# Optimization experiments

Measured on AMD Instinct MI355X. Metric: run time of the kernel, lower is better.

The kernel has to match this reference:

```python
import jax, jax.numpy as jnp
import numpy as np

D_IN = 128
D_OUT = 128
B, N = 8, 2048
NEG = -9e15


def setup_inputs() -> dict:
    key = jax.random.key(0)
    ks = jax.random.split(key, 7)
    x = jax.random.normal(ks[0], (B, N, D_IN), dtype=jnp.float32)
    adj = jax.random.randint(ks[1], (B, N, N), 0, 2).astype(jnp.float32)
    s_in = 1.0 / np.sqrt(D_IN)
    s_out = 1.0 / np.sqrt(D_OUT)
    s_g = 1.0 / np.sqrt(2 * D_OUT)
    # torch.nn.Linear weights stored pre-transposed: [in, out]
    W_w = jax.random.uniform(ks[2], (D_IN, D_OUT), jnp.float32, -s_in, s_in)
    W_b = jax.random.uniform(ks[3], (D_OUT,), jnp.float32, -s_in, s_in)
    A_w = jax.random.uniform(ks[4], (D_OUT, D_OUT), jnp.float32, -s_out, s_out)
    gate_w = jax.random.uniform(ks[5], (2 * D_OUT, 1), jnp.float32, -s_g, s_g)
    gate_b = jax.random.uniform(ks[6], (1,), jnp.float32, -s_g, s_g)
    return {"x": x, "adj": adj, "W_w": W_w, "W_b": W_b, "A_w": A_w,
            "gate_w": gate_w, "gate_b": gate_b}


def reference(x, adj, W_w, W_b, A_w, gate_w, gate_b):
    h = x @ W_w + W_b                                  # [B,N,D]
    e = jnp.einsum('bnd,bmd->bnm', h @ A_w, h)          # [B,N,N]
    e = e + jnp.swapaxes(e, 1, 2)                       # symmetric
    att = jnp.where(adj > 0, e, NEG)
    att = jax.nn.softmax(att, axis=1)                   # NOTE: dim=1 as in torch code
    att = att * adj
    h_prime = jax.nn.relu(jnp.einsum('bnm,bmd->bnd', att, h))
    coeff = jax.nn.sigmoid(jnp.concatenate([x, h_prime], axis=-1) @ gate_w + gate_b)  # [B,N,1]
    return coeff * x + (1.0 - coeff) * h_prime
```

## Files before the change

### kernel.cpp

```cpp
#include <hip/hip_runtime.h>
#include <hip/hip_bf16.h>

#define B_ 8
#define N_ 2048
#define D_ 128

typedef __bf16 bf16_t;
typedef __bf16 v8bf __attribute__((ext_vector_type(8)));
typedef float  v4f  __attribute__((ext_vector_type(4)));

__global__ __launch_bounds__(256) void k_prep(
    const float* __restrict__ Ww, const float* __restrict__ Aw,
    bf16_t* __restrict__ WT, bf16_t* __restrict__ AT)
{
    int idx = blockIdx.x * 256 + threadIdx.x;
    int o = idx >> 7, i = idx & 127;
    WT[idx] = (bf16_t)Ww[i * D_ + o];
    AT[idx] = (bf16_t)Aw[i * D_ + o];
}

__global__ __launch_bounds__(256) void k_hg(
    const float* __restrict__ x, const float* __restrict__ Wb,
    const bf16_t* __restrict__ WT, const bf16_t* __restrict__ AT,
    bf16_t* __restrict__ hb, bf16_t* __restrict__ gb)
{
    int wave = threadIdx.x >> 6;
    int lane = threadIdx.x & 63;
    int q = lane >> 4;
    int c = lane & 15;
    int nrow0 = blockIdx.x * 64 + wave * 16;

    __shared__ float pw_all[4][16][132];
    float (*pw)[132] = pw_all[wave];

    v8bf ax[4];
#pragma unroll
    for (int kc = 0; kc < 4; ++kc) {
        const float* src = x + (size_t)(nrow0 + c) * D_ + kc * 32 + q * 8;
        float4 f0 = *(const float4*)src;
        float4 f1 = *(const float4*)(src + 4);
        v8bf a;
        a[0]=(bf16_t)f0.x; a[1]=(bf16_t)f0.y; a[2]=(bf16_t)f0.z; a[3]=(bf16_t)f0.w;
        a[4]=(bf16_t)f1.x; a[5]=(bf16_t)f1.y; a[6]=(bf16_t)f1.z; a[7]=(bf16_t)f1.w;
        ax[kc] = a;
    }

#pragma unroll
    for (int ct = 0; ct < 8; ++ct) {
        float bias = Wb[ct * 16 + c];
        v4f acc = {bias, bias, bias, bias};
#pragma unroll
        for (int kc = 0; kc < 4; ++kc) {
            v8bf bw = *(const v8bf*)(WT + (size_t)(ct * 16 + c) * D_ + kc * 32 + q * 8);
            acc = __builtin_amdgcn_mfma_f32_16x16x32_bf16(ax[kc], bw, acc, 0, 0, 0);
        }
#pragma unroll
        for (int r = 0; r < 4; ++r) pw[q * 4 + r][ct * 16 + c] = acc[r];
    }
    __builtin_amdgcn_wave_barrier();

    v8bf ahf[4];
#pragma unroll
    for (int kc = 0; kc < 4; ++kc) {
        v4f p0 = *(const v4f*)&pw[c][kc * 32 + q * 8];
        v4f p1 = *(const v4f*)&pw[c][kc * 32 + q * 8 + 4];
        v8bf a;
#pragma unroll
        for (int j = 0; j < 4; ++j) { a[j] = (bf16_t)p0[j]; a[j+4] = (bf16_t)p1[j]; }
        ahf[kc] = a;
    }
    {
        int row = lane >> 2, seg = lane & 3;
#pragma unroll
        for (int v = 0; v < 4; ++v) {
            v8bf hv;
#pragma unroll
            for (int j = 0; j < 8; ++j) hv[j] = (bf16_t)pw[row][seg * 32 + v * 8 + j];
            *(v8bf*)(hb + (size_t)(nrow0 + row) * D_ + seg * 32 + v * 8) = hv;
        }
    }
    __builtin_amdgcn_wave_barrier();

#pragma unroll
    for (int ct = 0; ct < 8; ++ct) {
        v4f acc = {0.f, 0.f, 0.f, 0.f};
#pragma unroll
        for (int kc = 0; kc < 4; ++kc) {
            v8bf bw = *(const v8bf*)(AT + (size_t)(ct * 16 + c) * D_ + kc * 32 + q * 8);
            acc = __builtin_amdgcn_mfma_f32_16x16x32_bf16(ahf[kc], bw, acc, 0, 0, 0);
        }
#pragma unroll
        for (int r = 0; r < 4; ++r) pw[q * 4 + r][ct * 16 + c] = acc[r];
    }
    __builtin_amdgcn_wave_barrier();
    {
        int row = lane >> 2, seg = lane & 3;
#pragma unroll
        for (int v = 0; v < 4; ++v) {
            v8bf gv;
#pragma unroll
            for (int j = 0; j < 8; ++j) gv[j] = (bf16_t)pw[row][seg * 32 + v * 8 + j];
            *(v8bf*)(gb + (size_t)(nrow0 + row) * D_ + seg * 32 + v * 8) = gv;
        }
    }
}

__global__ __launch_bounds__(256, 4) void k_att(
    const bf16_t* __restrict__ hb, const bf16_t* __restrict__ gb,
    const float* __restrict__ adj, float* __restrict__ colsum,
    bf16_t* __restrict__ Pt)
{
    int bid = blockIdx.x;
    int b = bid & 7;
    int rest = bid >> 3;
    int nblk = rest >> 3;
    int mgrp = rest & 7;
    int wave = threadIdx.x >> 6;
    int lane = threadIdx.x & 63;
    int q = lane >> 4;
    int c = lane & 15;
    int nbase = nblk * 32;
    int mwav = mgrp * 256 + wave * 64;
    const size_t hgoff = (size_t)b * N_ * D_;
    const float* adjb = adj + (size_t)b * N_ * N_;

    __shared__ __align__(16) bf16_t eb_all[4][32][72];
    bf16_t (*eb)[72] = eb_all[wave];

    v8bf ag[2][4], ah[2][4];
#pragma unroll
    for (int sub = 0; sub < 2; ++sub)
#pragma unroll
        for (int kc = 0; kc < 4; ++kc) {
            size_t off = hgoff + (size_t)(nbase + sub * 16 + c) * D_ + kc * 32 + q * 8;
            ag[sub][kc] = *(const v8bf*)(gb + off);
            ah[sub][kc] = *(const v8bf*)(hb + off);
        }

    for (int t = 0; t < 4; ++t) {
        int mt = mwav + t * 16;
        float av[2][4];
#pragma unroll
        for (int sub = 0; sub < 2; ++sub)
#pragma unroll
            for (int r = 0; r < 4; ++r)
                av[sub][r] = adjb[(size_t)(nbase + sub * 16 + q * 4 + r) * N_ + mt + c];
        v8bf bh[4], bg[4];
#pragma unroll
        for (int kc = 0; kc < 4; ++kc) {
            size_t off = hgoff + (size_t)(mt + c) * D_ + kc * 32 + q * 8;
            bh[kc] = *(const v8bf*)(hb + off);
            bg[kc] = *(const v8bf*)(gb + off);
        }
        v4f e[2];
        e[0] = (v4f){0.f, 0.f, 0.f, 0.f};
        e[1] = (v4f){0.f, 0.f, 0.f, 0.f};
#pragma unroll
        for (int kc = 0; kc < 4; ++kc)
#pragma unroll
            for (int sub = 0; sub < 2; ++sub) {
                e[sub] = __builtin_amdgcn_mfma_f32_16x16x32_bf16(ag[sub][kc], bh[kc], e[sub], 0, 0, 0);
                e[sub] = __builtin_amdgcn_mfma_f32_16x16x32_bf16(ah[sub][kc], bg[kc], e[sub], 0, 0, 0);
            }
        float cs = 0.f;
#pragma unroll
        for (int sub = 0; sub < 2; ++sub)
#pragma unroll
            for (int r = 0; r < 4; ++r) {
                float ex = __expf(e[sub][r]);
                float pv = (av[sub][r] > 0.f) ? ex : 0.f;
                eb[sub * 16 + q * 4 + r][t * 16 + c] = (bf16_t)pv;
                cs += pv;
            }
        cs += __shfl_xor(cs, 16);
        cs += __shfl_xor(cs, 32);
        if (lane < 16) atomicAdd(&colsum[b * N_ + mt + lane], cs);
    }
    __builtin_amdgcn_wave_barrier();
    int prow = lane >> 3, pseg = lane & 7;
#pragma unroll
    for (int pass = 0; pass < 4; ++pass) {
        int row = pass * 8 + prow;
        v8bf o = *(const v8bf*)&eb[row][pseg * 8];
        *(v8bf*)(Pt + ((size_t)b * N_ + nbase + row) * N_ + mwav + pseg * 8) = o;
    }
}

__global__ __launch_bounds__(256) void k_scaleT(
    const bf16_t* __restrict__ hb, const float* __restrict__ colsum,
    bf16_t* __restrict__ hbTs)
{
    int bid = blockIdx.x;
    int b = bid >> 6;
    int rem = bid & 63;
    int nblk = rem >> 1;
    int dblk = rem & 1;
    int tid = threadIdx.x;
    __shared__ bf16_t sm[64][72];
    __shared__ float sinv[64];
    int n0 = nblk * 64, d0 = dblk * 64;
    int r = tid >> 3, cg = tid & 7;
#pragma unroll
    for (int rr = 0; rr < 2; ++rr) {
        int row = r + rr * 32;
        *(v8bf*)&sm[row][cg * 8] =
            *(const v8bf*)(hb + (size_t)(b * N_ + n0 + row) * D_ + d0 + cg * 8);
    }
    if (tid < 64) {
        float s = colsum[b * N_ + n0 + tid];
        sinv[tid] = (s > 0.f) ? 1.f / s : 0.f;
    }
    __syncthreads();
#pragma unroll
    for (int rr = 0; rr < 2; ++rr) {
        int dr = r + rr * 32;
        v8bf v;
#pragma unroll
        for (int jj = 0; jj < 8; ++jj)
            v[jj] = (bf16_t)((float)sm[cg * 8 + jj][dr] * sinv[cg * 8 + jj]);
        *(v8bf*)(hbTs + (size_t)(b * D_ + d0 + dr) * N_ + n0 + cg * 8) = v;
    }
}

__global__ __launch_bounds__(512, 4) void k_out(
    const bf16_t* __restrict__ Pt, const bf16_t* __restrict__ hbTs,
    const float* __restrict__ x, const float* __restrict__ gw,
    const float* __restrict__ gbias, float* __restrict__ out)
{
    int bid = blockIdx.x;
    int b = bid & 7;
    int nblk = bid >> 3;
    int tid = threadIdx.x;
    int wave = tid >> 6;
    int lane = tid & 63;
    int q = lane >> 4;
    int c = lane & 15;
    int nbase = nblk * 32;
    int m0 = wave * 256;

    __shared__ float hp[32][132];

    const bf16_t* hTb = hbTs + (size_t)b * D_ * N_;
    const bf16_t* Pb  = Pt + (size_t)b * N_ * N_;

    v4f acc[2][8];
#pragma unroll
    for (int sub = 0; sub < 2; ++sub)
#pragma unroll
        for (int dt = 0; dt < 8; ++dt) acc[sub][dt] = (v4f){0.f, 0.f, 0.f, 0.f};

    for (int ch = 0; ch < 8; ++ch) {
        int mch = m0 + ch * 32;
        v8bf a[2];
#pragma unroll
        for (int sub = 0; sub < 2; ++sub)
            a[sub] = *(const v8bf*)(Pb + (size_t)(nbase + sub * 16 + c) * N_ + mch + q * 8);
        v8bf vt[8];
#pragma unroll
        for (int dt = 0; dt < 8; ++dt)
            vt[dt] = *(const v8bf*)(hTb + (size_t)(dt * 16 + c) * N_ + mch + q * 8);
#pragma unroll
        for (int dt = 0; dt < 8; ++dt)
#pragma unroll
            for (int sub = 0; sub < 2; ++sub)
                acc[sub][dt] = __builtin_amdgcn_mfma_f32_16x16x32_bf16(a[sub], vt[dt], acc[sub][dt], 0, 0, 0);
    }

    if (wave == 0) {
#pragma unroll
        for (int sub = 0; sub < 2; ++sub)
#pragma unroll
            for (int dt = 0; dt < 8; ++dt)
#pragma unroll
                for (int r = 0; r < 4; ++r)
                    hp[sub * 16 + q * 4 + r][dt * 16 + c] = acc[sub][dt][r];
    }
    __syncthreads();
#pragma unroll
    for (int wv = 1; wv < 8; ++wv) {
        if (wave == wv) {
#pragma unroll
            for (int sub = 0; sub < 2; ++sub)
#pragma unroll
                for (int dt = 0; dt < 8; ++dt)
#pragma unroll
                    for (int r = 0; r < 4; ++r)
                        hp[sub * 16 + q * 4 + r][dt * 16 + c] += acc[sub][dt][r];
        }
        __syncthreads();
    }

    int row = tid >> 4;
    int seg = tid & 15;
    size_t g = (size_t)b * N_ + nbase + row;
    const float* xr = x + g * D_ + seg * 8;
    float4 xa = *(const float4*)xr;
    float4 xb = *(const float4*)(xr + 4);
    float hv[8];
#pragma unroll
    for (int j = 0; j < 8; ++j) hv[j] = fmaxf(hp[row][seg * 8 + j], 0.f);
    float part = xa.x * gw[seg*8+0] + xa.y * gw[seg*8+1] + xa.z * gw[seg*8+2] + xa.w * gw[seg*8+3]
               + xb.x * gw[seg*8+4] + xb.y * gw[seg*8+5] + xb.z * gw[seg*8+6] + xb.w * gw[seg*8+7];
#pragma unroll
    for (int j = 0; j < 8; ++j) part += hv[j] * gw[D_ + seg * 8 + j];
    part += __shfl_xor(part, 1);
    part += __shfl_xor(part, 2);
    part += __shfl_xor(part, 4);
    part += __shfl_xor(part, 8);
    float coeff = 1.f / (1.f + __expf(-(part + gbias[0])));
    float4 o0, o1;
    o0.x = coeff * xa.x + (1.f - coeff) * hv[0];
    o0.y = coeff * xa.y + (1.f - coeff) * hv[1];
    o0.z = coeff * xa.z + (1.f - coeff) * hv[2];
    o0.w = coeff * xa.w + (1.f - coeff) * hv[3];
    o1.x = coeff * xb.x + (1.f - coeff) * hv[4];
    o1.y = coeff * xb.y + (1.f - coeff) * hv[5];
    o1.z = coeff * xb.z + (1.f - coeff) * hv[6];
    o1.w = coeff * xb.w + (1.f - coeff) * hv[7];
    float* orow = out + g * D_ + seg * 8;
    *(float4*)orow = o0;
    *(float4*)(orow + 4) = o1;
}

extern "C" void kernel_launch(void* const* d_in, const int* in_sizes, int n_in,
                              void* d_out, int out_size, void* d_ws, size_t ws_size,
                              hipStream_t stream)
{
    const float* x     = (const float*)d_in[0];
    const float* adj   = (const float*)d_in[1];
    const float* Ww    = (const float*)d_in[2];
    const float* Wb    = (const float*)d_in[3];
    const float* Aw    = (const float*)d_in[4];
    const float* gw    = (const float*)d_in[5];
    const float* gbias = (const float*)d_in[6];
    float* out = (float*)d_out;

    char* ws = (char*)d_ws;
    bf16_t* hb     = (bf16_t*)(ws);
    bf16_t* gb     = (bf16_t*)(ws + (4 << 20));
    bf16_t* hbTs   = (bf16_t*)(ws + (8 << 20));
    float*  colsum = (float*)(ws + (12 << 20));
    bf16_t* Pt     = (bf16_t*)(ws + (17 << 20));
    bf16_t* WT     = (bf16_t*)(ws + (81 << 20));
    bf16_t* AT     = (bf16_t*)(ws + (81 << 20) + (32 << 10));

    hipMemsetAsync(colsum, 0, B_ * N_ * sizeof(float), stream);
    k_prep<<<64, 256, 0, stream>>>(Ww, Aw, WT, AT);
    k_hg<<<B_ * N_ / 64, 256, 0, stream>>>(x, Wb, WT, AT, hb, gb);
    k_att<<<4096, 256, 0, stream>>>(hb, gb, adj, colsum, Pt);
    k_scaleT<<<512, 256, 0, stream>>>(hb, colsum, hbTs);
    k_out<<<512, 512, 0, stream>>>(Pt, hbTs, x, gw, gbias, out);
}
```

Baseline: 358.9 us.

## Enlarge attention tile, prefetch B operands, and coalesce adjacency loads

Each block now covers 64 n-rows instead of 32, so every loaded column tile of h/g feeds twice as many MFMAs and the grid halves. The next m-tile's h/g operands are prefetched into registers while the current tile computes. Adjacency masking and column-sum accumulation move into the write-out phase, which reads adj as float4 in coalesced rows and makes fewer, wider atomic adds. The cost is more registers per thread (launch bounds lowered to 2 blocks per SM) and twice the shared memory, so occupancy drops.

```diff
diff --git a/kernel.cpp b/kernel.cpp
--- a/kernel.cpp
+++ b/kernel.cpp
@@ -8,6 +8,9 @@
 typedef __bf16 bf16_t;
 typedef __bf16 v8bf __attribute__((ext_vector_type(8)));
 typedef float  v4f  __attribute__((ext_vector_type(4)));
+
+template <typename T>
+__device__ __forceinline__ void pinv(T& x) { asm volatile("" : "+v"(x)); }
 
 __global__ __launch_bounds__(256) void k_prep(
     const float* __restrict__ Ww, const float* __restrict__ Aw,
@@ -105,7 +108,7 @@
     }
 }
 
-__global__ __launch_bounds__(256, 4) void k_att(
+__global__ __launch_bounds__(256, 2) void k_att(
     const bf16_t* __restrict__ hb, const bf16_t* __restrict__ gb,
     const float* __restrict__ adj, float* __restrict__ colsum,
     bf16_t* __restrict__ Pt)
@@ -119,70 +122,97 @@
     int lane = threadIdx.x & 63;
     int q = lane >> 4;
     int c = lane & 15;
-    int nbase = nblk * 32;
+    int nbase = nblk * 64;
     int mwav = mgrp * 256 + wave * 64;
     const size_t hgoff = (size_t)b * N_ * D_;
     const float* adjb = adj + (size_t)b * N_ * N_;
 
-    __shared__ __align__(16) bf16_t eb_all[4][32][72];
+    __shared__ __align__(16) bf16_t eb_all[4][64][72];
     bf16_t (*eb)[72] = eb_all[wave];
 
-    v8bf ag[2][4], ah[2][4];
-#pragma unroll
-    for (int sub = 0; sub < 2; ++sub)
+    v8bf ag[4][4], ah[4][4];
+#pragma unroll
+    for (int sub = 0; sub < 4; ++sub)
 #pragma unroll
         for (int kc = 0; kc < 4; ++kc) {
             size_t off = hgoff + (size_t)(nbase + sub * 16 + c) * D_ + kc * 32 + q * 8;
             ag[sub][kc] = *(const v8bf*)(gb + off);
             ah[sub][kc] = *(const v8bf*)(hb + off);
         }
+#pragma unroll
+    for (int sub = 0; sub < 4; ++sub)
+#pragma unroll
+        for (int kc = 0; kc < 4; ++kc) { pinv(ag[sub][kc]); pinv(ah[sub][kc]); }
+
+    v8bf bh[4], bg[4], bhn[4], bgn[4];
+#pragma unroll
+    for (int kc = 0; kc < 4; ++kc) {
+        size_t off = hgoff + (size_t)(mwav + c) * D_ + kc * 32 + q * 8;
+        bh[kc] = *(const v8bf*)(hb + off);
+        bg[kc] = *(const v8bf*)(gb + off);
+    }
 
     for (int t = 0; t < 4; ++t) {
-        int mt = mwav + t * 16;
-        float av[2][4];
-#pragma unroll
-        for (int sub = 0; sub < 2; ++sub)
-#pragma unroll
-            for (int r = 0; r < 4; ++r)
-                av[sub][r] = adjb[(size_t)(nbase + sub * 16 + q * 4 + r) * N_ + mt + c];
-        v8bf bh[4], bg[4];
-#pragma unroll
-        for (int kc = 0; kc < 4; ++kc) {
-            size_t off = hgoff + (size_t)(mt + c) * D_ + kc * 32 + q * 8;
-            bh[kc] = *(const v8bf*)(hb + off);
-            bg[kc] = *(const v8bf*)(gb + off);
-        }
-        v4f e[2];
-        e[0] = (v4f){0.f, 0.f, 0.f, 0.f};
-        e[1] = (v4f){0.f, 0.f, 0.f, 0.f};
+        if (t < 3) {
+            int mt = mwav + (t + 1) * 16;
+#pragma unroll
+            for (int kc = 0; kc < 4; ++kc) {
+                size_t off = hgoff + (size_t)(mt + c) * D_ + kc * 32 + q * 8;
+                bhn[kc] = *(const v8bf*)(hb + off);
+                bgn[kc] = *(const v8bf*)(gb + off);
+            }
+        }
+        v4f e[4];
+#pragma unroll
+        for (int sub = 0; sub < 4; ++sub) e[sub] = (v4f){0.f, 0.f, 0.f, 0.f};
 #pragma unroll
         for (int kc = 0; kc < 4; ++kc)
 #pragma unroll
-            for (int sub = 0; sub < 2; ++sub) {
+            for (int sub = 0; sub < 4; ++sub) {
                 e[sub] = __builtin_amdgcn_mfma_f32_16x16x32_bf16(ag[sub][kc], bh[kc], e[sub], 0, 0, 0);
                 e[sub] = __builtin_amdgcn_mfma_f32_16x16x32_bf16(ah[sub][kc], bg[kc], e[sub], 0, 0, 0);
             }
-        float cs = 0.f;
-#pragma unroll
-        for (int sub = 0; sub < 2; ++sub)
-#pragma unroll
-            for (int r = 0; r < 4; ++r) {
-                float ex = __expf(e[sub][r]);
-                float pv = (av[sub][r] > 0.f) ? ex : 0.f;
-                eb[sub * 16 + q * 4 + r][t * 16 + c] = (bf16_t)pv;
-                cs += pv;
-            }
-        cs += __shfl_xor(cs, 16);
-        cs += __shfl_xor(cs, 32);
-        if (lane < 16) atomicAdd(&colsum[b * N_ + mt + lane], cs);
+#pragma unroll
+        for (int sub = 0; sub < 4; ++sub)
+#pragma unroll
+            for (int r = 0; r < 4; ++r)
+                eb[sub * 16 + q * 4 + r][t * 16 + c] = (bf16_t)__expf(e[sub][r]);
+#pragma unroll
+        for (int kc = 0; kc < 4; ++kc) { bh[kc] = bhn[kc]; bg[kc] = bgn[kc]; }
     }
     __builtin_amdgcn_wave_barrier();
+
     int prow = lane >> 3, pseg = lane & 7;
-#pragma unroll
-    for (int pass = 0; pass < 4; ++pass) {
+    float cs[8];
+#pragma unroll
+    for (int j = 0; j < 8; ++j) cs[j] = 0.f;
+#pragma unroll
+    for (int pass = 0; pass < 8; ++pass) {
         int row = pass * 8 + prow;
-        v8bf o = *(const v8bf*)&eb[row][pseg * 8];
+        v8bf e8 = *(const v8bf*)&eb[row][pseg * 8];
+        const float* ap = adjb + (size_t)(nbase + row) * N_ + mwav + pseg * 8;
+        float4 a0 = *(const float4*)ap;
+        float4 a1 = *(const float4*)(ap + 4);
+        float am[8] = {a0.x, a0.y, a0.z, a0.w, a1.x, a1.y, a1.z, a1.w};
+        v8bf o;
+#pragma unroll
+        for (int j = 0; j < 8; ++j) {
+            bool live = am[j] > 0.f;
+            o[j] = live ? e8[j] : (bf16_t)0.f;
+            cs[j] += live ? (float)e8[j] : 0.f;
+        }
         *(v8bf*)(Pt + ((size_t)b * N_ + nbase + row) * N_ + mwav + pseg * 8) = o;
+    }
+#pragma unroll
+    for (int j = 0; j < 8; ++j) {
+        cs[j] += __shfl_xor(cs[j], 8);
+        cs[j] += __shfl_xor(cs[j], 16);
+        cs[j] += __shfl_xor(cs[j], 32);
+    }
+    if (lane < 8) {
+#pragma unroll
+        for (int j = 0; j < 8; ++j)
+            atomicAdd(&colsum[b * N_ + mwav + lane * 8 + j], cs[j]);
     }
 }
 
@@ -347,7 +377,7 @@
     hipMemsetAsync(colsum, 0, B_ * N_ * sizeof(float), stream);
     k_prep<<<64, 256, 0, stream>>>(Ww, Aw, WT, AT);
     k_hg<<<B_ * N_ / 64, 256, 0, stream>>>(x, Wb, WT, AT, hb, gb);
-    k_att<<<4096, 256, 0, stream>>>(hb, gb, adj, colsum, Pt);
+    k_att<<<2048, 256, 0, stream>>>(hb, gb, adj, colsum, Pt);
     k_scaleT<<<512, 256, 0, stream>>>(hb, colsum, hbTs);
     k_out<<<512, 512, 0, stream>>>(Pt, hbTs, x, gw, gbias, out);
 }
```

Result: faster. 332.1 us (-7.5%).

## Double k_att row tile with LDS-staged operands and prefetch next column tile

Applied to the files above, without the earlier changes.

k_att now handles 64 n-rows per block instead of 32, stages those rows' h and g tiles in shared memory, and prefetches the next 16-column h/g fragment while computing the current one. This halves the grid and reuses each loaded m-side fragment across more rows, at the cost of LDS reads inside the MFMA loop and lower occupancy (launch bounds 4 to 3). Pt is now written directly from registers as scattered 2-byte stores rather than via an LDS transpose with 16-byte stores, which may hurt write coalescing. k_hg is also restructured into 512-thread blocks of 32 rows, with waves splitting the output columns and block-level syncs.

```diff
diff --git a/kernel.cpp b/kernel.cpp
--- a/kernel.cpp
+++ b/kernel.cpp
@@ -19,24 +19,27 @@
     AT[idx] = (bf16_t)Aw[i * D_ + o];
 }
 
-__global__ __launch_bounds__(256) void k_hg(
+__global__ __launch_bounds__(512) void k_hg(
     const float* __restrict__ x, const float* __restrict__ Wb,
     const bf16_t* __restrict__ WT, const bf16_t* __restrict__ AT,
     bf16_t* __restrict__ hb, bf16_t* __restrict__ gb)
 {
-    int wave = threadIdx.x >> 6;
-    int lane = threadIdx.x & 63;
+    int tid = threadIdx.x;
+    int lane = tid & 63;
+    int wave = tid >> 6;
     int q = lane >> 4;
     int c = lane & 15;
-    int nrow0 = blockIdx.x * 64 + wave * 16;
-
-    __shared__ float pw_all[4][16][132];
-    float (*pw)[132] = pw_all[wave];
+    int rg = wave & 1;
+    int dh = wave >> 1;
+    int row0 = blockIdx.x * 32;
+    int nrow = row0 + rg * 16;
+
+    __shared__ float hs[32][132];
 
     v8bf ax[4];
 #pragma unroll
     for (int kc = 0; kc < 4; ++kc) {
-        const float* src = x + (size_t)(nrow0 + c) * D_ + kc * 32 + q * 8;
+        const float* src = x + (size_t)(nrow + c) * D_ + kc * 32 + q * 8;
         float4 f0 = *(const float4*)src;
         float4 f1 = *(const float4*)(src + 4);
         v8bf a;
@@ -46,7 +49,8 @@
     }
 
 #pragma unroll
-    for (int ct = 0; ct < 8; ++ct) {
+    for (int t = 0; t < 2; ++t) {
+        int ct = dh * 2 + t;
         float bias = Wb[ct * 16 + c];
         v4f acc = {bias, bias, bias, bias};
 #pragma unroll
@@ -55,57 +59,62 @@
             acc = __builtin_amdgcn_mfma_f32_16x16x32_bf16(ax[kc], bw, acc, 0, 0, 0);
         }
 #pragma unroll
-        for (int r = 0; r < 4; ++r) pw[q * 4 + r][ct * 16 + c] = acc[r];
-    }
-    __builtin_amdgcn_wave_barrier();
+        for (int r = 0; r < 4; ++r) hs[rg * 16 + q * 4 + r][ct * 16 + c] = acc[r];
+    }
+    __syncthreads();
 
     v8bf ahf[4];
 #pragma unroll
     for (int kc = 0; kc < 4; ++kc) {
-        v4f p0 = *(const v4f*)&pw[c][kc * 32 + q * 8];
-        v4f p1 = *(const v4f*)&pw[c][kc * 32 + q * 8 + 4];
+        v4f p0 = *(const v4f*)&hs[rg * 16 + c][kc * 32 + q * 8];
+        v4f p1 = *(const v4f*)&hs[rg * 16 + c][kc * 32 + q * 8 + 4];
         v8bf a;
 #pragma unroll
         for (int j = 0; j < 4; ++j) { a[j] = (bf16_t)p0[j]; a[j+4] = (bf16_t)p1[j]; }
         ahf[kc] = a;
     }
     {
-        int row = lane >> 2, seg = lane & 3;
-#pragma unroll
-        for (int v = 0; v < 4; ++v) {
-            v8bf hv;
-#pragma unroll
-            for (int j = 0; j < 8; ++j) hv[j] = (bf16_t)pw[row][seg * 32 + v * 8 + j];
-            *(v8bf*)(hb + (size_t)(nrow0 + row) * D_ + seg * 32 + v * 8) = hv;
-        }
-    }
-    __builtin_amdgcn_wave_barrier();
-
-#pragma unroll
-    for (int ct = 0; ct < 8; ++ct) {
+        int r2 = tid >> 4, s = tid & 15;
+        v4f p0 = *(const v4f*)&hs[r2][s * 8];
+        v4f p1 = *(const v4f*)&hs[r2][s * 8 + 4];
+        v8bf hv;
+#pragma unroll
+        for (int j = 0; j < 4; ++j) { hv[j] = (bf16_t)p0[j]; hv[j+4] = (bf16_t)p1[j]; }
+        *(v8bf*)(hb + (size_t)(row0 + r2) * D_ + s * 8) = hv;
+    }
+
+    v4f gacc[2];
+#pragma unroll
+    for (int t = 0; t < 2; ++t) {
+        int ct = dh * 2 + t;
         v4f acc = {0.f, 0.f, 0.f, 0.f};
 #pragma unroll
         for (int kc = 0; kc < 4; ++kc) {
             v8bf bw = *(const v8bf*)(AT + (size_t)(ct * 16 + c) * D_ + kc * 32 + q * 8);
             acc = __builtin_amdgcn_mfma_f32_16x16x32_bf16(ahf[kc], bw, acc, 0, 0, 0);
         }
-#pragma unroll
-        for (int r = 0; r < 4; ++r) pw[q * 4 + r][ct * 16 + c] = acc[r];
-    }
-    __builtin_amdgcn_wave_barrier();
+        gacc[t] = acc;
+    }
+    __syncthreads();
+#pragma unroll
+    for (int t = 0; t < 2; ++t) {
+        int ct = dh * 2 + t;
+#pragma unroll
+        for (int r = 0; r < 4; ++r) hs[rg * 16 + q * 4 + r][ct * 16 + c] = gacc[t][r];
+    }
+    __syncthreads();
     {
-        int row = lane >> 2, seg = lane & 3;
-#pragma unroll
-        for (int v = 0; v < 4; ++v) {
-            v8bf gv;
-#pragma unroll
-            for (int j = 0; j < 8; ++j) gv[j] = (bf16_t)pw[row][seg * 32 + v * 8 + j];
-            *(v8bf*)(gb + (size_t)(nrow0 + row) * D_ + seg * 32 + v * 8) = gv;
-        }
-    }
-}
-
-__global__ __launch_bounds__(256, 4) void k_att(
+        int r2 = tid >> 4, s = tid & 15;
+        v4f p0 = *(const v4f*)&hs[r2][s * 8];
+        v4f p1 = *(const v4f*)&hs[r2][s * 8 + 4];
+        v8bf gv;
+#pragma unroll
+        for (int j = 0; j < 4; ++j) { gv[j] = (bf16_t)p0[j]; gv[j+4] = (bf16_t)p1[j]; }
+        *(v8bf*)(gb + (size_t)(row0 + r2) * D_ + s * 8) = gv;
+    }
+}
+
+__global__ __launch_bounds__(256, 3) void k_att(
     const bf16_t* __restrict__ hb, const bf16_t* __restrict__ gb,
     const float* __restrict__ adj, float* __restrict__ colsum,
     bf16_t* __restrict__ Pt)
@@ -115,74 +124,82 @@
     int rest = bid >> 3;
     int nblk = rest >> 3;
     int mgrp = rest & 7;
-    int wave = threadIdx.x >> 6;
-    int lane = threadIdx.x & 63;
+    int tid = threadIdx.x;
+    int wave = tid >> 6;
+    int lane = tid & 63;
     int q = lane >> 4;
     int c = lane & 15;
-    int nbase = nblk * 32;
+    int nbase = nblk * 64;
     int mwav = mgrp * 256 + wave * 64;
     const size_t hgoff = (size_t)b * N_ * D_;
     const float* adjb = adj + (size_t)b * N_ * N_;
 
-    __shared__ __align__(16) bf16_t eb_all[4][32][72];
-    bf16_t (*eb)[72] = eb_all[wave];
-
-    v8bf ag[2][4], ah[2][4];
-#pragma unroll
-    for (int sub = 0; sub < 2; ++sub)
-#pragma unroll
-        for (int kc = 0; kc < 4; ++kc) {
-            size_t off = hgoff + (size_t)(nbase + sub * 16 + c) * D_ + kc * 32 + q * 8;
-            ag[sub][kc] = *(const v8bf*)(gb + off);
-            ah[sub][kc] = *(const v8bf*)(hb + off);
-        }
+    __shared__ __align__(16) bf16_t hs[64][136];
+    __shared__ __align__(16) bf16_t gs[64][136];
+
+    {
+        int r = tid >> 2, seg = tid & 3;
+        const bf16_t* hsrc = hb + hgoff + (size_t)(nbase + r) * D_ + seg * 32;
+        const bf16_t* gsrc = gb + hgoff + (size_t)(nbase + r) * D_ + seg * 32;
+#pragma unroll
+        for (int v = 0; v < 4; ++v) {
+            *(v8bf*)&hs[r][seg * 32 + v * 8] = *(const v8bf*)(hsrc + v * 8);
+            *(v8bf*)&gs[r][seg * 32 + v * 8] = *(const v8bf*)(gsrc + v * 8);
+        }
+    }
+    __syncthreads();
+
+    v8bf bh[4], bg[4], bhn[4], bgn[4];
+#pragma unroll
+    for (int kc = 0; kc < 4; ++kc) {
+        size_t off = hgoff + (size_t)(mwav + c) * D_ + kc * 32 + q * 8;
+        bh[kc] = *(const v8bf*)(hb + off);
+        bg[kc] = *(const v8bf*)(gb + off);
+    }
 
     for (int t = 0; t < 4; ++t) {
         int mt = mwav + t * 16;
-        float av[2][4];
-#pragma unroll
-        for (int sub = 0; sub < 2; ++sub)
+        float av[4][4];
+#pragma unroll
+        for (int sub = 0; sub < 4; ++sub)
 #pragma unroll
             for (int r = 0; r < 4; ++r)
                 av[sub][r] = adjb[(size_t)(nbase + sub * 16 + q * 4 + r) * N_ + mt + c];
-        v8bf bh[4], bg[4];
-#pragma unroll
-        for (int kc = 0; kc < 4; ++kc) {
-            size_t off = hgoff + (size_t)(mt + c) * D_ + kc * 32 + q * 8;
-            bh[kc] = *(const v8bf*)(hb + off);
-            bg[kc] = *(const v8bf*)(gb + off);
-        }
-        v4f e[2];
-        e[0] = (v4f){0.f, 0.f, 0.f, 0.f};
-        e[1] = (v4f){0.f, 0.f, 0.f, 0.f};
+        if (t < 3) {
+#pragma unroll
+            for (int kc = 0; kc < 4; ++kc) {
+                size_t off = hgoff + (size_t)(mt + 16 + c) * D_ + kc * 32 + q * 8;
+                bhn[kc] = *(const v8bf*)(hb + off);
+                bgn[kc] = *(const v8bf*)(gb + off);
+            }
+        }
+        v4f e[4];
+#pragma unroll
+        for (int sub = 0; sub < 4; ++sub) e[sub] = (v4f){0.f, 0.f, 0.f, 0.f};
 #pragma unroll
         for (int kc = 0; kc < 4; ++kc)
 #pragma unroll
-            for (int sub = 0; sub < 2; ++sub) {
-                e[sub] = __builtin_amdgcn_mfma_f32_16x16x32_bf16(ag[sub][kc], bh[kc], e[sub], 0, 0, 0);
-                e[sub] = __builtin_amdgcn_mfma_f32_16x16x32_bf16(ah[sub][kc], bg[kc], e[sub], 0, 0, 0);
+            for (int sub = 0; sub < 4; ++sub) {
+                v8bf ag = *(const v8bf*)&gs[sub * 16 + c][kc * 32 + q * 8];
+                v8bf ah = *(const v8bf*)&hs[sub * 16 + c][kc * 32 + q * 8];
+                e[sub] = __builtin_amdgcn_mfma_f32_16x16x32_bf16(ag, bh[kc], e[sub], 0, 0, 0);
+                e[sub] = __builtin_amdgcn_mfma_f32_16x16x32_bf16(ah, bg[kc], e[sub], 0, 0, 0);
             }
         float cs = 0.f;
 #pragma unroll
-        for (int sub = 0; sub < 2; ++sub)
+        for (int sub = 0; sub < 4; ++sub)
 #pragma unroll
             for (int r = 0; r < 4; ++r) {
                 float ex = __expf(e[sub][r]);
                 float pv = (av[sub][r] > 0.f) ? ex : 0.f;
-                eb[sub * 16 + q * 4 + r][t * 16 + c] = (bf16_t)pv;
                 cs += pv;
+                Pt[((size_t)b * N_ + nbase + sub * 16 + q * 4 + r) * N_ + mt + c] = (bf16_t)pv;
             }
         cs += __shfl_xor(cs, 16);
         cs += __shfl_xor(cs, 32);
         if (lane < 16) atomicAdd(&colsum[b * N_ + mt + lane], cs);
-    }
-    __builtin_amdgcn_wave_barrier();
-    int prow = lane >> 3, pseg = lane & 7;
-#pragma unroll
-    for (int pass = 0; pass < 4; ++pass) {
-        int row = pass * 8 + prow;
-        v8bf o = *(const v8bf*)&eb[row][pseg * 8];
-        *(v8bf*)(Pt + ((size_t)b * N_ + nbase + row) * N_ + mwav + pseg * 8) = o;
+#pragma unroll
+        for (int kc = 0; kc < 4; ++kc) { bh[kc] = bhn[kc]; bg[kc] = bgn[kc]; }
     }
 }
 
@@ -346,8 +363,8 @@
 
     hipMemsetAsync(colsum, 0, B_ * N_ * sizeof(float), stream);
     k_prep<<<64, 256, 0, stream>>>(Ww, Aw, WT, AT);
-    k_hg<<<B_ * N_ / 64, 256, 0, stream>>>(x, Wb, WT, AT, hb, gb);
-    k_att<<<4096, 256, 0, stream>>>(hb, gb, adj, colsum, Pt);
+    k_hg<<<B_ * N_ / 32, 512, 0, stream>>>(x, Wb, WT, AT, hb, gb);
+    k_att<<<2048, 256, 0, stream>>>(hb, gb, adj, colsum, Pt);
     k_scaleT<<<512, 256, 0, stream>>>(hb, colsum, hbTs);
     k_out<<<512, 512, 0, stream>>>(Pt, hbTs, x, gw, gbias, out);
 }
```

Result: faster. 336.6 us (-6.2%).
